# Kernel tuning notes

Hardware: AMD Instinct MI355X
Metric: run time of the kernel (lower is better)

The kernel has to match this reference:

```python
import jax, jax.numpy as jnp
import numpy as np

B, CIN, COUT = 4, 32, 32
D1, D2, D3 = 64, 64, 64
M1, M2, M3 = 32, 32, 17  # n_modes with last dim -> 32//2+1 after rfft redundancy
INIT_STD = (2.0 / (CIN + COUT)) ** 0.5


def setup_inputs() -> dict:
    key = jax.random.key(0)
    k_x, k_wr, k_wi, k_b = jax.random.split(key, 4)
    x = jax.random.normal(k_x, (B, CIN, D1, D2, D3), dtype=jnp.float32)
    # ComplexDense factorized weight, normal_(0, init_std) on real and imag parts
    w_real = INIT_STD * jax.random.normal(k_wr, (CIN, COUT, M1, M2, M3), dtype=jnp.float32)
    w_imag = INIT_STD * jax.random.normal(k_wi, (CIN, COUT, M1, M2, M3), dtype=jnp.float32)
    # bias: (n_layers=1, out_channels, 1, 1, 1); we take index 0 slice
    bias = INIT_STD * jax.random.normal(k_b, (1, COUT, 1, 1, 1), dtype=jnp.float32)
    return {"x": x, "w_real": w_real, "w_imag": w_imag, "bias": bias}


def reference(x, w_real, w_imag, bias):
    fft_axes = (-3, -2, -1)
    b, cin, d1, d2, d3 = x.shape
    f3 = d3 // 2 + 1
    # forward rFFT, shift all but last (real) axis so low modes are centered
    xf = jnp.fft.rfftn(x, axes=fft_axes)               # (B, Cin, D1, D2, f3) complex
    xf = jnp.fft.fftshift(xf, axes=fft_axes[:-1])
    weight = w_real + 1j * w_imag                       # (Cin, Cout, M1, M2, M3)
    m1, m2, m3 = weight.shape[2:]
    s1, s2 = (d1 - m1) // 2, (d2 - m2) // 2
    xs = xf[:, :, s1:s1 + m1, s2:s2 + m2, :m3]          # centered low modes
    # channel contraction in Fourier space: abcde,bfcde->afcde
    out_modes = jnp.einsum('abcde,bfcde->afcde', xs, weight)
    out_fft = jnp.zeros((b, weight.shape[1], d1, d2, f3), dtype=out_modes.dtype)
    out_fft = out_fft.at[:, :, s1:s1 + m1, s2:s2 + m2, :m3].set(out_modes)
    # torch applies fftshift (not ifftshift); identical for even sizes
    out_fft = jnp.fft.fftshift(out_fft, axes=fft_axes[:-1])
    out = jnp.fft.irfftn(out_fft, s=(d1, d2, d3), axes=fft_axes)
    return out + bias[0]
```

## Files before the change

kernel.cpp:

```cpp
#include <hip/hip_runtime.h>
#include <math.h>

static constexpr int NB  = 4;
static constexpr int NC  = 32;

__device__ __attribute__((aligned(256))) float T3F[64 * 48];
__device__ __attribute__((aligned(256))) float2 T3I2[17 * 64];
__device__ __attribute__((aligned(256))) float T12F[64 * 64];
__device__ __attribute__((aligned(256))) float TINV[32 * 128];

__global__ __launch_bounds__(256) void k0_init() {
    const int t = blockIdx.x * 256 + threadIdx.x;
    if (t < 64 * 17) {
        int n = t / 17, k = t % 17;
        int idx = (n * k) & 63;
        float s, c;
        sincospif(idx / 32.0f, &s, &c);
        T3F[n * 48 + 2 * k] = c;  T3F[n * 48 + 2 * k + 1] = -s;
    }
    if (t < 64) {
        for (int q = 34; q < 48; ++q) T3F[t * 48 + q] = 0.f;
    }
    if (t < 17 * 64) {
        int k = t >> 6, n = t & 63;
        int idx = (n * k) & 63;
        float s, c;
        sincospif(idx / 32.0f, &s, &c);
        T3I2[t] = make_float2(c, s);
    }
    if (t < 64 * 32) {
        int n = t / 32, p = t % 32;
        int o = (p + 48) & 63;
        int idx = (o * n) & 63;
        float s, c;
        sincospif(idx / 32.0f, &s, &c);
        T12F[n * 64 + 2 * p] = c;  T12F[n * 64 + 2 * p + 1] = -s;
    }
    if (t < 32 * 64) {
        int p = t / 64, n = t % 64;
        int o = (p + 48) & 63;
        int idx = (o * n) & 63;
        float s, c;
        sincospif(idx / 32.0f, &s, &c);
        TINV[p * 128 + 2 * n] = c;  TINV[p * 128 + 2 * n + 1] = s;
    }
}

__device__ __forceinline__ void cmadd(float2& a, float2 x, float wx, float wy) {
    a.x = fmaf(x.x, wx, fmaf(-x.y, wy, a.x));
    a.y = fmaf(x.x, wy, fmaf( x.y, wx, a.y));
}

__global__ __launch_bounds__(64)
void k1_rfft_d3(const float* __restrict__ x, float2* __restrict__ o1) {
    __shared__ float tile[64 * 65];
    const int t = threadIdx.x, bid = blockIdx.x;
    const float4* src4 = (const float4*)(x + (size_t)bid * 4096);
    for (int j = 0; j < 16; ++j) {
        int f4 = j * 64 + t;
        float4 v = src4[f4];
        int d2 = f4 >> 4, n0 = (f4 & 15) << 2;
        float* p = &tile[d2 * 65 + n0];
        p[0] = v.x; p[1] = v.y; p[2] = v.z; p[3] = v.w;
    }
    __syncthreads();
    float ar[17], ai[17];
#pragma unroll
    for (int k = 0; k < 17; ++k) { ar[k] = 0.f; ai[k] = 0.f; }
    const float* row = &tile[t * 65];
    for (int n = 0; n < 64; ++n) {
        float xv = row[n];
        const float* w = &T3F[n * 48];
#pragma unroll
        for (int k = 0; k < 17; ++k) {
            ar[k] = fmaf(xv, w[2 * k], ar[k]);
            ai[k] = fmaf(xv, w[2 * k + 1], ai[k]);
        }
    }
    const int bc = bid >> 6, d1 = bid & 63;
    float2* dst = o1 + (size_t)bc * (17 * 4096) + d1 * 64 + t;
#pragma unroll
    for (int k = 0; k < 17; ++k)
        dst[(size_t)k * 4096] = make_float2(ar[k], ai[k]);
}

__global__ __launch_bounds__(256)
void k2a_dft_d2(const float2* __restrict__ in, float2* __restrict__ T) {
    __shared__ float smem[8320];
    float* re = smem;
    float* im = smem + 64 * 65;
    const int t = threadIdx.x;
    const size_t base = (size_t)blockIdx.x * 4096;
    for (int j = 0; j < 16; ++j) {
        int idx = j * 256 + t;
        float2 v = in[base + idx];
        int d1 = idx >> 6, n2 = idx & 63;
        re[d1 * 65 + n2] = v.x;
        im[d1 * 65 + n2] = v.y;
    }
    __syncthreads();
    const int d1 = t & 63;
    const int pg = __builtin_amdgcn_readfirstlane(t >> 6);
    float2 acc[8];
#pragma unroll
    for (int j = 0; j < 8; ++j) acc[j] = make_float2(0.f, 0.f);
    const float* rrow = &re[d1 * 65];
    const float* irow = &im[d1 * 65];
#pragma unroll 2
    for (int n2 = 0; n2 < 64; ++n2) {
        float xr = rrow[n2], xi = irow[n2];
        const float* w = &T12F[n2 * 64 + pg * 16];
#pragma unroll
        for (int j = 0; j < 8; ++j)
            cmadd(acc[j], make_float2(xr, xi), w[2 * j], w[2 * j + 1]);
    }
    __syncthreads();
    float2* tile = (float2*)smem;
#pragma unroll
    for (int j = 0; j < 8; ++j) tile[d1 * 33 + pg * 8 + j] = acc[j];
    __syncthreads();
    float2* dst = T + (size_t)blockIdx.x * 2048;
#pragma unroll
    for (int q = 0; q < 8; ++q) {
        int e = t * 8 + q;
        dst[e] = tile[(e >> 5) * 33 + (e & 31)];
    }
}

__global__ __launch_bounds__(544)
void k2b_dft_d1(const float2* __restrict__ T, float2* __restrict__ Y) {
    __shared__ float2 tile[8 * 544];
    const int u = threadIdx.x;
    const int bc = blockIdx.x, pg = blockIdx.y;
    const int k3 = u >> 5, p2 = u & 31;
    const float2* src = T + ((size_t)bc * 17 + k3) * 2048 + p2;
    float2 acc[8];
#pragma unroll
    for (int j = 0; j < 8; ++j) acc[j] = make_float2(0.f, 0.f);
#pragma unroll 2
    for (int n1 = 0; n1 < 64; ++n1) {
        float2 xv = src[n1 * 32];
        const float* w = &T12F[n1 * 64 + pg * 16];
#pragma unroll
        for (int j = 0; j < 8; ++j)
            cmadd(acc[j], xv, w[2 * j], w[2 * j + 1]);
    }
#pragma unroll
    for (int j = 0; j < 8; ++j)
        tile[j * 544 + p2 * 17 + k3] = acc[j];
    __syncthreads();
    float2* dst = Y + (size_t)bc * 17408 + (size_t)pg * 8 * 544;
#pragma unroll
    for (int i = 0; i < 8; ++i)
        dst[u + i * 544] = tile[u + i * 544];
}

__global__ __launch_bounds__(64)
void k3_mix(const float2* __restrict__ Y, const float* __restrict__ wr,
            const float* __restrict__ wi, float2* __restrict__ Z) {
    const int m = blockIdx.x * 64 + threadIdx.x;
    const int ch = blockIdx.y;
    float2 acc[4][4];
#pragma unroll
    for (int a = 0; a < 4; ++a)
#pragma unroll
        for (int co = 0; co < 4; ++co) acc[a][co] = make_float2(0.f, 0.f);
#pragma unroll 8
    for (int cin = 0; cin < 32; ++cin) {
        float2 xv[4];
#pragma unroll
        for (int a = 0; a < 4; ++a)
            xv[a] = Y[((size_t)a * 32 + cin) * 17408 + m];
        size_t wb = ((size_t)cin * 32 + ch * 4) * 17408 + m;
#pragma unroll
        for (int co = 0; co < 4; ++co) {
            float wrv = wr[wb + (size_t)co * 17408];
            float wiv = wi[wb + (size_t)co * 17408];
#pragma unroll
            for (int a = 0; a < 4; ++a)
                cmadd(acc[a][co], xv[a], wrv, wiv);
        }
    }
#pragma unroll
    for (int a = 0; a < 4; ++a)
#pragma unroll
        for (int co = 0; co < 4; ++co)
            Z[((size_t)a * 32 + ch * 4 + co) * 17408 + m] = acc[a][co];
}

__global__ __launch_bounds__(544)
void k4a_idft_d1(const float2* __restrict__ Z, float2* __restrict__ U) {
    const int u = threadIdx.x;
    const int bf = blockIdx.x, ng = blockIdx.y;
    const float2* src = Z + (size_t)bf * 17408 + u;
    float2 acc[8];
#pragma unroll
    for (int j = 0; j < 8; ++j) acc[j] = make_float2(0.f, 0.f);
#pragma unroll 2
    for (int p1 = 0; p1 < 32; ++p1) {
        float2 xv = src[(size_t)p1 * 544];
        const float* w = &TINV[p1 * 128 + ng * 16];
#pragma unroll
        for (int j = 0; j < 8; ++j)
            cmadd(acc[j], xv, w[2 * j], w[2 * j + 1]);
    }
    float2* dst = U + (size_t)bf * 34816 + (size_t)ng * 8 * 544 + u;
#pragma unroll
    for (int j = 0; j < 8; ++j) dst[(size_t)j * 544] = acc[j];
}

__global__ __launch_bounds__(256, 4)
void k45w_ifft23(const float2* __restrict__ U, const float* __restrict__ bias,
                 float* __restrict__ out) {
    __shared__ __align__(16) float2 Ur[4][576];
    const int t = threadIdx.x;
    const int lane = t & 63;
    const int w = __builtin_amdgcn_readfirstlane(t >> 6);
    const int bf = blockIdx.x;
    const int n1 = blockIdx.y * 4 + w;
    float2* ur = Ur[w];
    float2 tws[32];
#pragma unroll
    for (int p = 0; p < 32; ++p)
        tws[p] = *(const float2*)&TINV[p * 128 + 2 * lane];
    const float2* src = U + (size_t)bf * 34816 + (size_t)n1 * 544;
    {
        int j = lane;
#pragma unroll
        for (int it = 0; it < 8; ++it) {
            float2 v = src[j];
            ur[(j / 17) * 18 + (j % 17)] = v;
            j += 64;
        }
        if (lane < 32) {
            int jj = 512 + lane;
            float2 v = src[jj];
            ur[(jj / 17) * 18 + (jj % 17)] = v;
        }
    }
    float2 X[17];
#pragma unroll
    for (int k = 0; k < 17; ++k) X[k] = make_float2(0.f, 0.f);
#pragma unroll
    for (int p2 = 0; p2 < 32; ++p2) {
        const float2* up = &ur[p2 * 18];
        const float c = tws[p2].x, s = tws[p2].y;
#pragma unroll
        for (int h = 0; h < 8; ++h) {
            float4 q = *(const float4*)&up[h * 2];
            X[2 * h].x     = fmaf(q.x, c, fmaf(-q.y, s, X[2 * h].x));
            X[2 * h].y     = fmaf(q.x, s, fmaf( q.y, c, X[2 * h].y));
            X[2 * h + 1].x = fmaf(q.z, c, fmaf(-q.w, s, X[2 * h + 1].x));
            X[2 * h + 1].y = fmaf(q.z, s, fmaf( q.w, c, X[2 * h + 1].y));
        }
        float2 qt = up[16];
        X[16].x = fmaf(qt.x, c, fmaf(-qt.y, s, X[16].x));
        X[16].y = fmaf(qt.x, s, fmaf( qt.y, c, X[16].y));
    }
    const float inv2 = 2.0f / 262144.0f;
#pragma unroll
    for (int k = 0; k < 17; ++k) { X[k].x *= inv2; X[k].y *= inv2; }
    const float bv = bias[bf & 31];
    float* dst = out + (size_t)bf * 262144 + (size_t)n1 * 4096 + (size_t)lane * 64;
#pragma unroll
    for (int nq = 0; nq < 16; ++nq) {
        float y0 = fmaf(X[0].x, 0.5f, bv);
        float y1 = y0, y2 = y0, y3 = y0;
#pragma unroll
        for (int k = 1; k < 17; ++k) {
            const float2* tr = &T3I2[k * 64 + nq * 4];
            float2 t0 = tr[0], t1 = tr[1], t2 = tr[2], t3 = tr[3];
            y0 = fmaf(X[k].x, t0.x, y0);  y0 = fmaf(-X[k].y, t0.y, y0);
            y1 = fmaf(X[k].x, t1.x, y1);  y1 = fmaf(-X[k].y, t1.y, y1);
            y2 = fmaf(X[k].x, t2.x, y2);  y2 = fmaf(-X[k].y, t2.y, y2);
            y3 = fmaf(X[k].x, t3.x, y3);  y3 = fmaf(-X[k].y, t3.y, y3);
        }
        *(float4*)&dst[nq * 4] = make_float4(y0, y1, y2, y3);
    }
}

extern "C" void kernel_launch(void* const* d_in, const int* in_sizes, int n_in,
                              void* d_out, int out_size, void* d_ws, size_t ws_size,
                              hipStream_t stream) {
    const float* x    = (const float*)d_in[0];
    const float* wr   = (const float*)d_in[1];
    const float* wi   = (const float*)d_in[2];
    const float* bias = (const float*)d_in[3];
    float* out = (float*)d_out;

    float2* A = (float2*)d_ws;
    float2* B = A + (size_t)2176 * 4096;
    float2* Y = A;
    float2* Z = A + (size_t)17825792 / 8;

    k0_init    <<<8, 256, 0, stream>>>();
    k1_rfft_d3 <<<NB * NC * 64, 64, 0, stream>>>(x, A);
    k2a_dft_d2 <<<2176, 256, 0, stream>>>(A, B);
    k2b_dft_d1 <<<dim3(128, 4), 544, 0, stream>>>(B, Y);
    k3_mix     <<<dim3(272, 8), 64, 0, stream>>>(Y, wr, wi, Z);
    k4a_idft_d1<<<dim3(128, 8), 544, 0, stream>>>(Z, B);
    k45w_ifft23<<<dim3(128, 16), 256, 0, stream>>>(B, bias, out);
}
```

Before: 303.3 us.

## Apply radix-2 splitting to the final inverse DFT stages along d2 and d3

The d2 inverse DFT in the last kernel now has each half-wave sum over only the even or the odd input rows, using a new 32-point twiddle table. The two halves are then combined with a cross-lane shuffle and a butterfly twiddle. The real d3 inverse transform uses the even/odd symmetry of the output index, so each computed pair of partial sums yields two output positions (n and n+32). This halves the loop count. Together these cut the FMA count of the dominant output kernel roughly in half. The cost is extra shuffles, a new init table, and different rounding order.

```diff
diff --git a/kernel.cpp b/kernel.cpp
--- a/kernel.cpp
+++ b/kernel.cpp
@@ -8,6 +8,7 @@
 __device__ __attribute__((aligned(256))) float2 T3I2[17 * 64];
 __device__ __attribute__((aligned(256))) float T12F[64 * 64];
 __device__ __attribute__((aligned(256))) float TINV[32 * 128];
+__device__ __attribute__((aligned(256))) float2 T32V[16 * 32];
 
 __global__ __launch_bounds__(256) void k0_init() {
     const int t = blockIdx.x * 256 + threadIdx.x;
@@ -43,6 +44,14 @@
         float s, c;
         sincospif(idx / 32.0f, &s, &c);
         TINV[p * 128 + 2 * n] = c;  TINV[p * 128 + 2 * n + 1] = s;
+    }
+    if (t < 16 * 32) {
+        int q = t >> 5, m = t & 31;
+        int j = (q + 24) & 31;
+        int idx = (j * m) & 31;
+        float s, c;
+        sincospif(idx / 16.0f, &s, &c);
+        T32V[t] = make_float2(c, s);
     }
 }
 
@@ -210,7 +219,7 @@
 }
 
 __global__ __launch_bounds__(256, 4)
-void k45w_ifft23(const float2* __restrict__ U, const float* __restrict__ bias,
+void k45r_ifft23(const float2* __restrict__ U, const float* __restrict__ bias,
                  float* __restrict__ out) {
     __shared__ __align__(16) float2 Ur[4][576];
     const int t = threadIdx.x;
@@ -219,10 +228,13 @@
     const int bf = blockIdx.x;
     const int n1 = blockIdx.y * 4 + w;
     float2* ur = Ur[w];
-    float2 tws[32];
-#pragma unroll
-    for (int p = 0; p < 32; ++p)
-        tws[p] = *(const float2*)&TINV[p * 128 + 2 * lane];
+    const int hi = lane >> 5;
+    const int m  = lane & 31;
+    float2 t32[16];
+#pragma unroll
+    for (int q = 0; q < 16; ++q)
+        t32[q] = T32V[q * 32 + m];
+    const float2 wv = T3I2[64 + lane];
     const float2* src = U + (size_t)bf * 34816 + (size_t)n1 * 544;
     {
         int j = lane;
@@ -238,44 +250,69 @@
             ur[(jj / 17) * 18 + (jj % 17)] = v;
         }
     }
-    float2 X[17];
-#pragma unroll
-    for (int k = 0; k < 17; ++k) X[k] = make_float2(0.f, 0.f);
-#pragma unroll
-    for (int p2 = 0; p2 < 32; ++p2) {
-        const float2* up = &ur[p2 * 18];
-        const float c = tws[p2].x, s = tws[p2].y;
+    float2 S[17];
+#pragma unroll
+    for (int k = 0; k < 17; ++k) S[k] = make_float2(0.f, 0.f);
+#pragma unroll
+    for (int q = 0; q < 16; ++q) {
+        const float2* up = &ur[(2 * q + hi) * 18];
+        const float c = t32[q].x, s = t32[q].y;
 #pragma unroll
         for (int h = 0; h < 8; ++h) {
-            float4 q = *(const float4*)&up[h * 2];
-            X[2 * h].x     = fmaf(q.x, c, fmaf(-q.y, s, X[2 * h].x));
-            X[2 * h].y     = fmaf(q.x, s, fmaf( q.y, c, X[2 * h].y));
-            X[2 * h + 1].x = fmaf(q.z, c, fmaf(-q.w, s, X[2 * h + 1].x));
-            X[2 * h + 1].y = fmaf(q.z, s, fmaf( q.w, c, X[2 * h + 1].y));
+            float4 qd = *(const float4*)&up[h * 2];
+            S[2 * h].x     = fmaf(qd.x, c, fmaf(-qd.y, s, S[2 * h].x));
+            S[2 * h].y     = fmaf(qd.x, s, fmaf( qd.y, c, S[2 * h].y));
+            S[2 * h + 1].x = fmaf(qd.z, c, fmaf(-qd.w, s, S[2 * h + 1].x));
+            S[2 * h + 1].y = fmaf(qd.z, s, fmaf( qd.w, c, S[2 * h + 1].y));
         }
         float2 qt = up[16];
-        X[16].x = fmaf(qt.x, c, fmaf(-qt.y, s, X[16].x));
-        X[16].y = fmaf(qt.x, s, fmaf( qt.y, c, X[16].y));
+        S[16].x = fmaf(qt.x, c, fmaf(-qt.y, s, S[16].x));
+        S[16].y = fmaf(qt.x, s, fmaf( qt.y, c, S[16].y));
     }
     const float inv2 = 2.0f / 262144.0f;
 #pragma unroll
-    for (int k = 0; k < 17; ++k) { X[k].x *= inv2; X[k].y *= inv2; }
+    for (int k = 0; k < 17; ++k) {
+        float px = __shfl_xor(S[k].x, 32);
+        float py = __shfl_xor(S[k].y, 32);
+        float ax = hi ? px : S[k].x;
+        float ay = hi ? py : S[k].y;
+        float bx = hi ? S[k].x : px;
+        float by = hi ? S[k].y : py;
+        S[k].x = fmaf(wv.x, bx, fmaf(-wv.y, by, ax)) * inv2;
+        S[k].y = fmaf(wv.x, by, fmaf( wv.y, bx, ay)) * inv2;
+    }
     const float bv = bias[bf & 31];
+    const float base = fmaf(S[0].x, 0.5f, bv);
     float* dst = out + (size_t)bf * 262144 + (size_t)n1 * 4096 + (size_t)lane * 64;
 #pragma unroll
-    for (int nq = 0; nq < 16; ++nq) {
-        float y0 = fmaf(X[0].x, 0.5f, bv);
-        float y1 = y0, y2 = y0, y3 = y0;
-#pragma unroll
-        for (int k = 1; k < 17; ++k) {
-            const float2* tr = &T3I2[k * 64 + nq * 4];
-            float2 t0 = tr[0], t1 = tr[1], t2 = tr[2], t3 = tr[3];
-            y0 = fmaf(X[k].x, t0.x, y0);  y0 = fmaf(-X[k].y, t0.y, y0);
-            y1 = fmaf(X[k].x, t1.x, y1);  y1 = fmaf(-X[k].y, t1.y, y1);
-            y2 = fmaf(X[k].x, t2.x, y2);  y2 = fmaf(-X[k].y, t2.y, y2);
-            y3 = fmaf(X[k].x, t3.x, y3);  y3 = fmaf(-X[k].y, t3.y, y3);
-        }
-        *(float4*)&dst[nq * 4] = make_float4(y0, y1, y2, y3);
+    for (int nq = 0; nq < 8; ++nq) {
+        float yE[4], yO[4];
+#pragma unroll
+        for (int r = 0; r < 4; ++r) { yE[r] = base; yO[r] = 0.f; }
+#pragma unroll
+        for (int j = 1; j <= 8; ++j) {
+            const float2* tr = &T3I2[(2 * j) * 64 + nq * 4];
+#pragma unroll
+            for (int r = 0; r < 4; ++r) {
+                float2 tw = tr[r];
+                yE[r] = fmaf(S[2 * j].x, tw.x, yE[r]);
+                yE[r] = fmaf(-S[2 * j].y, tw.y, yE[r]);
+            }
+        }
+#pragma unroll
+        for (int j = 0; j < 8; ++j) {
+            const float2* tr = &T3I2[(2 * j + 1) * 64 + nq * 4];
+#pragma unroll
+            for (int r = 0; r < 4; ++r) {
+                float2 tw = tr[r];
+                yO[r] = fmaf(S[2 * j + 1].x, tw.x, yO[r]);
+                yO[r] = fmaf(-S[2 * j + 1].y, tw.y, yO[r]);
+            }
+        }
+        *(float4*)&dst[nq * 4] =
+            make_float4(yE[0] + yO[0], yE[1] + yO[1], yE[2] + yO[2], yE[3] + yO[3]);
+        *(float4*)&dst[nq * 4 + 32] =
+            make_float4(yE[0] - yO[0], yE[1] - yO[1], yE[2] - yO[2], yE[3] - yO[3]);
     }
 }
 
@@ -299,5 +336,5 @@
     k2b_dft_d1 <<<dim3(128, 4), 544, 0, stream>>>(B, Y);
     k3_mix     <<<dim3(272, 8), 64, 0, stream>>>(Y, wr, wi, Z);
     k4a_idft_d1<<<dim3(128, 8), 544, 0, stream>>>(Z, B);
-    k45w_ifft23<<<dim3(128, 16), 256, 0, stream>>>(B, bias, out);
-}
+    k45r_ifft23<<<dim3(128, 16), 256, 0, stream>>>(B, bias, out);
+}
```

Result: no change. 309.2 us (+2.0%).
